# Kernel optimization log

Measured on AMD Instinct MI355X. Metric: run time of the kernel, lower is better.

The kernel has to match this reference:

```python
import jax, jax.numpy as jnp
import numpy as np

BASE_ALPHA = 0.05
NUM_ITER = 2
EPS = 1e-06


def setup_inputs() -> dict:
    key = jax.random.key(0)
    k1, k2 = jax.random.split(key)
    pred = jax.random.normal(k1, (8, 8192, 3), dtype=jnp.float32)
    partial = jax.random.normal(k2, (8, 2048, 3), dtype=jnp.float32)
    return {"pred": pred, "partial": partial}


def _cdist(a, b):
    # Euclidean pairwise distances via ||a||^2 - 2ab + ||b||^2 (avoids [B,N,M,3] temp).
    a2 = jnp.sum(a * a, axis=-1)  # [B,N]
    b2 = jnp.sum(b * b, axis=-1)  # [B,M]
    d2 = a2[:, :, None] - 2.0 * jnp.einsum('bnd,bmd->bnm', a, b) + b2[:, None, :]
    return jnp.sqrt(jnp.maximum(d2, 0.0))


def reference(pred, partial):
    refined = pred
    for _ in range(NUM_ITER):
        dist = _cdist(refined, partial)          # [B,N,M]
        min_dist = jnp.min(dist, axis=-1)        # [B,N]
        min_idx = jnp.argmin(dist, axis=-1)      # [B,N]
        nearest = jnp.take_along_axis(partial, min_idx[:, :, None], axis=1)  # [B,N,3]
        dist_norm = min_dist / (jnp.max(min_dist, axis=-1, keepdims=True) + EPS)
        alpha = BASE_ALPHA * (2.0 - dist_norm)   # [B,N]
        refined = refined + alpha[:, :, None] * (nearest - refined)
    return refined
```

## Files before the change

kernel.cpp:

```cpp
#include <hip/hip_runtime.h>
#include <math.h>

#define BATCH 8
#define NPRED 8192
#define MPART 2048
#define NPTS  (BATCH * NPRED)
#define MTOT  (BATCH * MPART)
#define QPL   4
#define SPLIT 16
#define PTS_PER_SPLIT (MPART / SPLIT)
#define GPS   (PTS_PER_SPLIT / 4)
#define QPB   256
#define NBLK  (NPTS / QPB)
#define BLK_PER_B (NPRED / QPB)
#define BASE_ALPHA 0.05f
#define EPS 1e-6f

__global__ __launch_bounds__(256) void prep_kernel(const float* __restrict__ partial,
                                                   float* __restrict__ ppgf,
                                                   float4* __restrict__ near4) {
    const int m = blockIdx.x * 256 + threadIdx.x;
    const float* p = partial + 3u * (unsigned)m;
    const float x = p[0], y = p[1], z = p[2];
    const int g = m >> 2, c = m & 3;
    float* base = ppgf + (size_t)g * 16 + c;
    base[0]  = -2.0f * x;
    base[4]  = -2.0f * y;
    base[8]  = -2.0f * z;
    base[12] = fmaf(x, x, fmaf(y, y, z * z));
    near4[m] = make_float4(x, y, z, 0.0f);
}

template <bool FUSE>
__global__ __launch_bounds__(1024) void nn_kernel(
    const float* __restrict__ src,
    const float4* __restrict__ ppg,
    const float4* __restrict__ near4,
    const float* md_in, const int* idx_in,
    const float* __restrict__ bmax_in,
    float* __restrict__ refined_out,
    float* md_out, int* idx_out,
    float* __restrict__ bmax_out)
{
    __shared__ float4 ldsP[2048];
    __shared__ float smax[4];
    unsigned long long* lk = (unsigned long long*)ldsP;

    const int qb   = blockIdx.x;
    const int b    = qb >> 5;
    const int tid  = threadIdx.x;
    const int wave = tid >> 6, lane = tid & 63;
    const int split = wave;

    const float4* gsrc = ppg + ((size_t)b << 11);
    ldsP[tid]        = gsrc[tid];
    ldsP[tid + 1024] = gsrc[tid + 1024];

    float axq[QPL], ayq[QPL], azq[QPL], a2q[QPL];
    if (FUSE) {
        float v = bmax_in[(b << 5) + (lane & 31)];
        #pragma unroll
        for (int o = 32; o > 0; o >>= 1) v = fmaxf(v, __shfl_down(v, o, 64));
        const float maxv = __shfl(v, 0, 64);
        #pragma unroll
        for (int j = 0; j < QPL; ++j) {
            const int t = (qb << 8) + (j << 6) + lane;
            const float md = md_in[t];
            const int   id = idx_in[t];
            const float alpha = BASE_ALPHA * (2.0f - md / (maxv + EPS));
            const float4 nb = near4[((size_t)b << 11) + id];
            const float* p = src + 3u * (unsigned)t;
            const float px = p[0], py = p[1], pz = p[2];
            axq[j] = fmaf(alpha, nb.x - px, px);
            ayq[j] = fmaf(alpha, nb.y - py, py);
            azq[j] = fmaf(alpha, nb.z - pz, pz);
            if (split == 0) {
                float* o = refined_out + 3u * (unsigned)t;
                o[0] = axq[j]; o[1] = ayq[j]; o[2] = azq[j];
            }
        }
    } else {
        #pragma unroll
        for (int j = 0; j < QPL; ++j) {
            const int t = (qb << 8) + (j << 6) + lane;
            const float* p = src + 3u * (unsigned)t;
            axq[j] = p[0]; ayq[j] = p[1]; azq[j] = p[2];
        }
    }
    #pragma unroll
    for (int j = 0; j < QPL; ++j)
        a2q[j] = fmaf(axq[j], axq[j], fmaf(ayq[j], ayq[j], azq[j] * azq[j]));

    __syncthreads();

    const float4* wp = ldsP + split * (GPS * 4);
    float best[QPL]; int bg[QPL];
    #pragma unroll
    for (int j = 0; j < QPL; ++j) { best[j] = 1e30f; bg[j] = 0; }

    #pragma unroll 2
    for (int i = 0; i < GPS; ++i) {
        const float4 X = wp[4 * i + 0];
        const float4 Y = wp[4 * i + 1];
        const float4 Z = wp[4 * i + 2];
        const float4 W = wp[4 * i + 3];
        #pragma unroll
        for (int j = 0; j < QPL; ++j) {
            const float ax = axq[j], ay = ayq[j], az = azq[j];
            const float d0 = fmaf(Z.x, az, fmaf(Y.x, ay, X.x * ax)) + W.x;
            const float d1 = fmaf(Z.y, az, fmaf(Y.y, ay, X.y * ax)) + W.y;
            const float d2 = fmaf(Z.z, az, fmaf(Y.z, ay, X.z * ax)) + W.z;
            const float d3 = fmaf(Z.w, az, fmaf(Y.w, ay, X.w * ax)) + W.w;
            const float gm = fminf(fminf(fminf(d0, d1), d2), d3);
            if (gm < best[j]) bg[j] = i;
            best[j] = fminf(best[j], gm);
        }
    }

    unsigned long long key[QPL];
    #pragma unroll
    for (int j = 0; j < QPL; ++j) {
        const int gi = bg[j];
        const float4 X = wp[4 * gi + 0];
        const float4 Y = wp[4 * gi + 1];
        const float4 Z = wp[4 * gi + 2];
        const float4 W = wp[4 * gi + 3];
        const float ax = axq[j], ay = ayq[j], az = azq[j];
        const float d0 = fmaf(Z.x, az, fmaf(Y.x, ay, X.x * ax)) + W.x;
        const float d1 = fmaf(Z.y, az, fmaf(Y.y, ay, X.y * ax)) + W.y;
        const float d2 = fmaf(Z.z, az, fmaf(Y.z, ay, X.z * ax)) + W.z;
        const float bv = best[j];
        int c;
        if      (d0 == bv) c = 0;
        else if (d1 == bv) c = 1;
        else if (d2 == bv) c = 2;
        else               c = 3;
        const int m = (split << 7) + (gi << 2) + c;
        const float dd = fmaxf(bv + a2q[j], 0.0f);
        key[j] = ((unsigned long long)__float_as_uint(dd) << 32) | (unsigned)m;
    }

    __syncthreads();
    #pragma unroll
    for (int j = 0; j < QPL; ++j)
        lk[split * QPB + (j << 6) + lane] = key[j];
    __syncthreads();

    if (wave < 4) {
        const int q2 = (wave << 6) + lane;
        unsigned long long kk = lk[q2];
        #pragma unroll
        for (int s = 1; s < SPLIT; ++s) {
            const unsigned long long k = lk[s * QPB + q2];
            if (k < kk) kk = k;
        }
        const float md = sqrtf(__uint_as_float((unsigned)(kk >> 32)));
        const int t2 = (qb << 8) + q2;
        md_out[t2]  = md;
        idx_out[t2] = (int)(kk & 0xffffffffu);
        float w = md;
        #pragma unroll
        for (int o = 32; o > 0; o >>= 1) w = fmaxf(w, __shfl_down(w, o, 64));
        if (lane == 0) smax[wave] = w;
    }
    __syncthreads();
    if (tid == 0)
        bmax_out[qb] = fmaxf(fmaxf(smax[0], smax[1]), fmaxf(smax[2], smax[3]));
}

__global__ __launch_bounds__(256) void update_kernel(
    const float* __restrict__ refined1,
    const float4* __restrict__ near4,
    const float* __restrict__ md2,
    const int*   __restrict__ idx2,
    const float* __restrict__ bmax2,
    float* __restrict__ out)
{
    const int t = blockIdx.x * 256 + threadIdx.x;
    const int b = t >> 13;
    const int lane = threadIdx.x & 63;
    float v = bmax2[(b << 5) + (lane & 31)];
    #pragma unroll
    for (int o = 32; o > 0; o >>= 1) v = fmaxf(v, __shfl_down(v, o, 64));
    const float maxv = __shfl(v, 0, 64);
    const float md = md2[t];
    const int   id = idx2[t];
    const float alpha = BASE_ALPHA * (2.0f - md / (maxv + EPS));
    const float4 nb = near4[((size_t)b << 11) + id];
    const float* p = refined1 + 3u * (unsigned)t;
    const float px = p[0], py = p[1], pz = p[2];
    float* o = out + 3u * (unsigned)t;
    o[0] = fmaf(alpha, nb.x - px, px);
    o[1] = fmaf(alpha, nb.y - py, py);
    o[2] = fmaf(alpha, nb.z - pz, pz);
}

extern "C" void kernel_launch(void* const* d_in, const int* in_sizes, int n_in,
                              void* d_out, int out_size, void* d_ws, size_t ws_size,
                              hipStream_t stream) {
    const float* pred    = (const float*)d_in[0];
    const float* partial = (const float*)d_in[1];
    float* out = (float*)d_out;

    char* ws = (char*)d_ws;
    float4* ppg   = (float4*)ws;
    float4* near4 = (float4*)(ws + 262144);
    float*  ref1  = (float*)(ws + 524288);
    float*  md1   = (float*)(ws + 1310720);
    int*    idx1  = (int*)(ws + 1572864);
    float*  bmax1 = (float*)(ws + 1835008);
    float*  bmax2 = bmax1 + NBLK;

    prep_kernel<<<MTOT / 256, 256, 0, stream>>>(partial, (float*)ppg, near4);

    nn_kernel<false><<<NBLK, 1024, 0, stream>>>(
        pred, ppg, near4, nullptr, nullptr, nullptr, nullptr, md1, idx1, bmax1);

    nn_kernel<true><<<NBLK, 1024, 0, stream>>>(
        pred, ppg, near4, md1, idx1, bmax1, ref1, md1, idx1, bmax2);

    update_kernel<<<NPTS / 256, 256, 0, stream>>>(ref1, near4, md1, idx1, bmax2, out);
}
```

Measured before the change: 99.25 us.

## Split NN search across two half-tile blocks and add key-combine kernel

Each nearest-neighbour block now uses 512 threads and scans half of the partial-cloud points, so twice as many smaller blocks run with a smaller LDS tile. A launch bound asks for four blocks per CU to raise occupancy. Per-half packed distance/index keys go to global memory, and a new combine kernel takes the min and computes per-block max distances. This adds two extra launches and a key round trip through global memory in exchange for better occupancy and load balance. The distance arithmetic is also refolded into a pure FMA chain with a tree min.

```diff
diff --git a/kernel.cpp b/kernel.cpp
--- a/kernel.cpp
+++ b/kernel.cpp
@@ -7,12 +7,11 @@
 #define NPTS  (BATCH * NPRED)
 #define MTOT  (BATCH * MPART)
 #define QPL   4
-#define SPLIT 16
-#define PTS_PER_SPLIT (MPART / SPLIT)
-#define GPS   (PTS_PER_SPLIT / 4)
 #define QPB   256
-#define NBLK  (NPTS / QPB)
-#define BLK_PER_B (NPRED / QPB)
+#define WAVES 8
+#define GPW   32
+#define NNBLK (2 * NPTS / QPB)
+#define NCMB  (NPTS / 1024)
 #define BASE_ALPHA 0.05f
 #define EPS 1e-6f
 
@@ -32,33 +31,32 @@
 }
 
 template <bool FUSE>
-__global__ __launch_bounds__(1024) void nn_kernel(
+__global__ __launch_bounds__(512, 4) void nn_kernel(
     const float* __restrict__ src,
     const float4* __restrict__ ppg,
     const float4* __restrict__ near4,
-    const float* md_in, const int* idx_in,
+    const float* __restrict__ md_in,
+    const int*   __restrict__ idx_in,
     const float* __restrict__ bmax_in,
-    float* __restrict__ refined_out,
-    float* md_out, int* idx_out,
-    float* __restrict__ bmax_out)
+    float* __restrict__ ref_out,
+    unsigned long long* __restrict__ keys_out)
 {
-    __shared__ float4 ldsP[2048];
-    __shared__ float smax[4];
-    unsigned long long* lk = (unsigned long long*)ldsP;
-
-    const int qb   = blockIdx.x;
+    __shared__ float4 tile[1024];
+    unsigned long long* lk = (unsigned long long*)tile;
+
+    const int qb   = blockIdx.x >> 1;
+    const int half = blockIdx.x & 1;
     const int b    = qb >> 5;
     const int tid  = threadIdx.x;
     const int wave = tid >> 6, lane = tid & 63;
-    const int split = wave;
-
-    const float4* gsrc = ppg + ((size_t)b << 11);
-    ldsP[tid]        = gsrc[tid];
-    ldsP[tid + 1024] = gsrc[tid + 1024];
+
+    const float4* gsrc = ppg + ((b << 11) + (half << 10));
+    tile[tid]       = gsrc[tid];
+    tile[tid + 512] = gsrc[tid + 512];
 
     float axq[QPL], ayq[QPL], azq[QPL], a2q[QPL];
     if (FUSE) {
-        float v = bmax_in[(b << 5) + (lane & 31)];
+        float v = bmax_in[(b << 3) + (lane & 7)];
         #pragma unroll
         for (int o = 32; o > 0; o >>= 1) v = fmaxf(v, __shfl_down(v, o, 64));
         const float maxv = __shfl(v, 0, 64);
@@ -68,14 +66,14 @@
             const float md = md_in[t];
             const int   id = idx_in[t];
             const float alpha = BASE_ALPHA * (2.0f - md / (maxv + EPS));
-            const float4 nb = near4[((size_t)b << 11) + id];
+            const float4 nb = near4[(b << 11) + id];
             const float* p = src + 3u * (unsigned)t;
             const float px = p[0], py = p[1], pz = p[2];
             axq[j] = fmaf(alpha, nb.x - px, px);
             ayq[j] = fmaf(alpha, nb.y - py, py);
             azq[j] = fmaf(alpha, nb.z - pz, pz);
-            if (split == 0) {
-                float* o = refined_out + 3u * (unsigned)t;
+            if (half == 0 && wave == 0) {
+                float* o = ref_out + 3u * (unsigned)t;
                 o[0] = axq[j]; o[1] = ayq[j]; o[2] = azq[j];
             }
         }
@@ -93,13 +91,13 @@
 
     __syncthreads();
 
-    const float4* wp = ldsP + split * (GPS * 4);
+    const float4* wp = tile + (wave << 7);
     float best[QPL]; int bg[QPL];
     #pragma unroll
     for (int j = 0; j < QPL; ++j) { best[j] = 1e30f; bg[j] = 0; }
 
-    #pragma unroll 2
-    for (int i = 0; i < GPS; ++i) {
+    #pragma unroll 4
+    for (int i = 0; i < GPW; ++i) {
         const float4 X = wp[4 * i + 0];
         const float4 Y = wp[4 * i + 1];
         const float4 Z = wp[4 * i + 2];
@@ -107,11 +105,11 @@
         #pragma unroll
         for (int j = 0; j < QPL; ++j) {
             const float ax = axq[j], ay = ayq[j], az = azq[j];
-            const float d0 = fmaf(Z.x, az, fmaf(Y.x, ay, X.x * ax)) + W.x;
-            const float d1 = fmaf(Z.y, az, fmaf(Y.y, ay, X.y * ax)) + W.y;
-            const float d2 = fmaf(Z.z, az, fmaf(Y.z, ay, X.z * ax)) + W.z;
-            const float d3 = fmaf(Z.w, az, fmaf(Y.w, ay, X.w * ax)) + W.w;
-            const float gm = fminf(fminf(fminf(d0, d1), d2), d3);
+            const float d0 = fmaf(Z.x, az, fmaf(Y.x, ay, fmaf(X.x, ax, W.x)));
+            const float d1 = fmaf(Z.y, az, fmaf(Y.y, ay, fmaf(X.y, ax, W.y)));
+            const float d2 = fmaf(Z.z, az, fmaf(Y.z, ay, fmaf(X.z, ax, W.z)));
+            const float d3 = fmaf(Z.w, az, fmaf(Y.w, ay, fmaf(X.w, ax, W.w)));
+            const float gm = fminf(fminf(d0, d1), fminf(d2, d3));
             if (gm < best[j]) bg[j] = i;
             best[j] = fminf(best[j], gm);
         }
@@ -126,16 +124,16 @@
         const float4 Z = wp[4 * gi + 2];
         const float4 W = wp[4 * gi + 3];
         const float ax = axq[j], ay = ayq[j], az = azq[j];
-        const float d0 = fmaf(Z.x, az, fmaf(Y.x, ay, X.x * ax)) + W.x;
-        const float d1 = fmaf(Z.y, az, fmaf(Y.y, ay, X.y * ax)) + W.y;
-        const float d2 = fmaf(Z.z, az, fmaf(Y.z, ay, X.z * ax)) + W.z;
+        const float d0 = fmaf(Z.x, az, fmaf(Y.x, ay, fmaf(X.x, ax, W.x)));
+        const float d1 = fmaf(Z.y, az, fmaf(Y.y, ay, fmaf(X.y, ax, W.y)));
+        const float d2 = fmaf(Z.z, az, fmaf(Y.z, ay, fmaf(X.z, ax, W.z)));
         const float bv = best[j];
         int c;
         if      (d0 == bv) c = 0;
         else if (d1 == bv) c = 1;
         else if (d2 == bv) c = 2;
         else               c = 3;
-        const int m = (split << 7) + (gi << 2) + c;
+        const int m = (half << 10) + (wave << 7) + (gi << 2) + c;
         const float dd = fmaxf(bv + a2q[j], 0.0f);
         key[j] = ((unsigned long long)__float_as_uint(dd) << 32) | (unsigned)m;
     }
@@ -143,33 +141,49 @@
     __syncthreads();
     #pragma unroll
     for (int j = 0; j < QPL; ++j)
-        lk[split * QPB + (j << 6) + lane] = key[j];
+        lk[wave * QPB + (j << 6) + lane] = key[j];
     __syncthreads();
 
     if (wave < 4) {
         const int q2 = (wave << 6) + lane;
         unsigned long long kk = lk[q2];
         #pragma unroll
-        for (int s = 1; s < SPLIT; ++s) {
+        for (int s = 1; s < WAVES; ++s) {
             const unsigned long long k = lk[s * QPB + q2];
             if (k < kk) kk = k;
         }
-        const float md = sqrtf(__uint_as_float((unsigned)(kk >> 32)));
-        const int t2 = (qb << 8) + q2;
-        md_out[t2]  = md;
-        idx_out[t2] = (int)(kk & 0xffffffffu);
-        float w = md;
-        #pragma unroll
-        for (int o = 32; o > 0; o >>= 1) w = fmaxf(w, __shfl_down(w, o, 64));
-        if (lane == 0) smax[wave] = w;
-    }
-    __syncthreads();
-    if (tid == 0)
-        bmax_out[qb] = fmaxf(fmaxf(smax[0], smax[1]), fmaxf(smax[2], smax[3]));
+        keys_out[half * NPTS + (qb << 8) + q2] = kk;
+    }
+}
+
+__global__ __launch_bounds__(1024) void combine_kernel(
+    const unsigned long long* __restrict__ keys,
+    float* __restrict__ md_out, int* __restrict__ idx_out,
+    float* __restrict__ bmax_out)
+{
+    __shared__ float smax[16];
+    const int t = blockIdx.x * 1024 + threadIdx.x;
+    const int wave = threadIdx.x >> 6, lane = threadIdx.x & 63;
+    const unsigned long long k0 = keys[t], k1 = keys[NPTS + t];
+    const unsigned long long kk = (k1 < k0) ? k1 : k0;
+    const float md = sqrtf(__uint_as_float((unsigned)(kk >> 32)));
+    md_out[t]  = md;
+    idx_out[t] = (int)(kk & 0xffffffffu);
+    float w = md;
+    #pragma unroll
+    for (int o = 32; o > 0; o >>= 1) w = fmaxf(w, __shfl_down(w, o, 64));
+    if (lane == 0) smax[wave] = w;
+    __syncthreads();
+    if (threadIdx.x < 64) {
+        float v = smax[lane & 15];
+        #pragma unroll
+        for (int o = 32; o > 0; o >>= 1) v = fmaxf(v, __shfl_down(v, o, 64));
+        if (lane == 0) bmax_out[blockIdx.x] = v;
+    }
 }
 
 __global__ __launch_bounds__(256) void update_kernel(
-    const float* __restrict__ refined1,
+    const float* __restrict__ ref1,
     const float4* __restrict__ near4,
     const float* __restrict__ md2,
     const int*   __restrict__ idx2,
@@ -179,15 +193,15 @@
     const int t = blockIdx.x * 256 + threadIdx.x;
     const int b = t >> 13;
     const int lane = threadIdx.x & 63;
-    float v = bmax2[(b << 5) + (lane & 31)];
+    float v = bmax2[(b << 3) + (lane & 7)];
     #pragma unroll
     for (int o = 32; o > 0; o >>= 1) v = fmaxf(v, __shfl_down(v, o, 64));
     const float maxv = __shfl(v, 0, 64);
     const float md = md2[t];
     const int   id = idx2[t];
     const float alpha = BASE_ALPHA * (2.0f - md / (maxv + EPS));
-    const float4 nb = near4[((size_t)b << 11) + id];
-    const float* p = refined1 + 3u * (unsigned)t;
+    const float4 nb = near4[(b << 11) + id];
+    const float* p = ref1 + 3u * (unsigned)t;
     const float px = p[0], py = p[1], pz = p[2];
     float* o = out + 3u * (unsigned)t;
     o[0] = fmaf(alpha, nb.x - px, px);
@@ -208,16 +222,19 @@
     float*  ref1  = (float*)(ws + 524288);
     float*  md1   = (float*)(ws + 1310720);
     int*    idx1  = (int*)(ws + 1572864);
-    float*  bmax1 = (float*)(ws + 1835008);
-    float*  bmax2 = bmax1 + NBLK;
+    unsigned long long* keys = (unsigned long long*)(ws + 1835008);
+    float*  bmax1 = (float*)(ws + 2883584);
+    float*  bmax2 = bmax1 + NCMB;
 
     prep_kernel<<<MTOT / 256, 256, 0, stream>>>(partial, (float*)ppg, near4);
 
-    nn_kernel<false><<<NBLK, 1024, 0, stream>>>(
-        pred, ppg, near4, nullptr, nullptr, nullptr, nullptr, md1, idx1, bmax1);
-
-    nn_kernel<true><<<NBLK, 1024, 0, stream>>>(
-        pred, ppg, near4, md1, idx1, bmax1, ref1, md1, idx1, bmax2);
+    nn_kernel<false><<<NNBLK, 512, 0, stream>>>(
+        pred, ppg, near4, nullptr, nullptr, nullptr, nullptr, keys);
+    combine_kernel<<<NCMB, 1024, 0, stream>>>(keys, md1, idx1, bmax1);
+
+    nn_kernel<true><<<NNBLK, 512, 0, stream>>>(
+        pred, ppg, near4, md1, idx1, bmax1, ref1, keys);
+    combine_kernel<<<NCMB, 1024, 0, stream>>>(keys, md1, idx1, bmax2);
 
     update_kernel<<<NPTS / 256, 256, 0, stream>>>(ref1, near4, md1, idx1, bmax2, out);
 }
```

Measured after the change: 100.7 us. No clear change (+1.4%).

## Fuse both NN iterations and final update into one cooperative kernel with grid sync

Applied to the files above, without the earlier changes.

Replaces the two nn_kernel launches and the update kernel with a single cooperative kernel. It keeps the partial tile and the refined query points resident in LDS and registers, and uses grid.sync for the per-batch max reductions. This removes two kernel launches and the global round-trips for md/idx/refined intermediates. It requires all 256 blocks of 1024 threads to be co-resident (launch_bounds 1024,4) and adds grid-wide barrier cost. LDS use per block rises to 64KB.

```diff
diff --git a/kernel.cpp b/kernel.cpp
--- a/kernel.cpp
+++ b/kernel.cpp
@@ -1,18 +1,14 @@
 #include <hip/hip_runtime.h>
+#include <hip/hip_cooperative_groups.h>
 #include <math.h>
+
+namespace cg = cooperative_groups;
 
 #define BATCH 8
 #define NPRED 8192
 #define MPART 2048
 #define NPTS  (BATCH * NPRED)
 #define MTOT  (BATCH * MPART)
-#define QPL   4
-#define SPLIT 16
-#define PTS_PER_SPLIT (MPART / SPLIT)
-#define GPS   (PTS_PER_SPLIT / 4)
-#define QPB   256
-#define NBLK  (NPTS / QPB)
-#define BLK_PER_B (NPRED / QPB)
 #define BASE_ALPHA 0.05f
 #define EPS 1e-6f
 
@@ -31,168 +27,165 @@
     near4[m] = make_float4(x, y, z, 0.0f);
 }
 
-template <bool FUSE>
-__global__ __launch_bounds__(1024) void nn_kernel(
-    const float* __restrict__ src,
+__global__ __launch_bounds__(1024, 4) void fused_kernel(
+    const float* __restrict__ pred,
     const float4* __restrict__ ppg,
     const float4* __restrict__ near4,
-    const float* md_in, const int* idx_in,
-    const float* __restrict__ bmax_in,
-    float* __restrict__ refined_out,
-    float* md_out, int* idx_out,
-    float* __restrict__ bmax_out)
+    float* __restrict__ bp1,
+    float* __restrict__ bp2,
+    float* __restrict__ out)
 {
-    __shared__ float4 ldsP[2048];
-    __shared__ float smax[4];
-    unsigned long long* lk = (unsigned long long*)ldsP;
+    cg::grid_group grid = cg::this_grid();
+
+    __shared__ float4 tile[2048];
+    __shared__ unsigned long long lk[4096];
 
     const int qb   = blockIdx.x;
     const int b    = qb >> 5;
     const int tid  = threadIdx.x;
     const int wave = tid >> 6, lane = tid & 63;
-    const int split = wave;
-
-    const float4* gsrc = ppg + ((size_t)b << 11);
-    ldsP[tid]        = gsrc[tid];
-    ldsP[tid + 1024] = gsrc[tid + 1024];
-
-    float axq[QPL], ayq[QPL], azq[QPL], a2q[QPL];
-    if (FUSE) {
-        float v = bmax_in[(b << 5) + (lane & 31)];
+
+    const float4* gsrc = ppg + (b << 11);
+    tile[tid]        = gsrc[tid];
+    tile[tid + 1024] = gsrc[tid + 1024];
+
+    float ax[4], ay[4], az[4], a2[4];
+    #pragma unroll
+    for (int j = 0; j < 4; ++j) {
+        const int t = (qb << 8) + (j << 6) + lane;
+        const float* p = pred + 3u * (unsigned)t;
+        ax[j] = p[0]; ay[j] = p[1]; az[j] = p[2];
+        a2[j] = fmaf(ax[j], ax[j], fmaf(ay[j], ay[j], az[j] * az[j]));
+    }
+    __syncthreads();
+
+    const float4* wp = tile + (wave << 7);
+
+    auto scan_keys = [&](unsigned long long* key) {
+        float best[4]; int bg[4];
+        #pragma unroll
+        for (int j = 0; j < 4; ++j) { best[j] = 1e30f; bg[j] = 0; }
+        #pragma unroll 4
+        for (int i = 0; i < 32; ++i) {
+            const float4 X = wp[4 * i + 0];
+            const float4 Y = wp[4 * i + 1];
+            const float4 Z = wp[4 * i + 2];
+            const float4 W = wp[4 * i + 3];
+            #pragma unroll
+            for (int j = 0; j < 4; ++j) {
+                const float d0 = fmaf(Z.x, az[j], fmaf(Y.x, ay[j], fmaf(X.x, ax[j], W.x)));
+                const float d1 = fmaf(Z.y, az[j], fmaf(Y.y, ay[j], fmaf(X.y, ax[j], W.y)));
+                const float d2 = fmaf(Z.z, az[j], fmaf(Y.z, ay[j], fmaf(X.z, ax[j], W.z)));
+                const float d3 = fmaf(Z.w, az[j], fmaf(Y.w, ay[j], fmaf(X.w, ax[j], W.w)));
+                const float gm = fminf(fminf(d0, d1), fminf(d2, d3));
+                if (gm < best[j]) bg[j] = i;
+                best[j] = fminf(best[j], gm);
+            }
+        }
+        #pragma unroll
+        for (int j = 0; j < 4; ++j) {
+            const int gi = bg[j];
+            const float4 X = wp[4 * gi + 0];
+            const float4 Y = wp[4 * gi + 1];
+            const float4 Z = wp[4 * gi + 2];
+            const float4 W = wp[4 * gi + 3];
+            const float d0 = fmaf(Z.x, az[j], fmaf(Y.x, ay[j], fmaf(X.x, ax[j], W.x)));
+            const float d1 = fmaf(Z.y, az[j], fmaf(Y.y, ay[j], fmaf(X.y, ax[j], W.y)));
+            const float d2 = fmaf(Z.z, az[j], fmaf(Y.z, ay[j], fmaf(X.z, ax[j], W.z)));
+            const float bv = best[j];
+            int c;
+            if      (d0 == bv) c = 0;
+            else if (d1 == bv) c = 1;
+            else if (d2 == bv) c = 2;
+            else               c = 3;
+            const int m = (wave << 7) + (gi << 2) + c;
+            const float dd = fmaxf(bv + a2[j], 0.0f);
+            key[j] = ((unsigned long long)__float_as_uint(dd) << 32) | (unsigned)m;
+        }
+    };
+
+    unsigned long long key1[4];
+    scan_keys(key1);
+    #pragma unroll
+    for (int j = 0; j < 4; ++j)
+        lk[(wave << 8) + (j << 6) + lane] = key1[j];
+    __syncthreads();
+
+    if (tid < 256) {
+        unsigned long long kk = lk[tid];
+        #pragma unroll
+        for (int s = 1; s < 16; ++s) {
+            const unsigned long long k = lk[(s << 8) + tid];
+            if (k < kk) kk = k;
+        }
+        lk[tid] = kk;
+        float w = sqrtf(__uint_as_float((unsigned)(kk >> 32)));
+        #pragma unroll
+        for (int o = 32; o > 0; o >>= 1) w = fmaxf(w, __shfl_down(w, o, 64));
+        if (lane == 0) bp1[(qb << 2) + wave] = w;
+    }
+    grid.sync();
+
+    {
+        float v = fmaxf(bp1[(b << 7) + lane], bp1[(b << 7) + 64 + lane]);
         #pragma unroll
         for (int o = 32; o > 0; o >>= 1) v = fmaxf(v, __shfl_down(v, o, 64));
         const float maxv = __shfl(v, 0, 64);
-        #pragma unroll
-        for (int j = 0; j < QPL; ++j) {
-            const int t = (qb << 8) + (j << 6) + lane;
-            const float md = md_in[t];
-            const int   id = idx_in[t];
+
+        #pragma unroll
+        for (int j = 0; j < 4; ++j) {
+            const int q = (j << 6) + lane;
+            const unsigned long long kk = lk[q];
+            const float md = sqrtf(__uint_as_float((unsigned)(kk >> 32)));
+            const int   id = (int)(kk & 0xffffffffu);
             const float alpha = BASE_ALPHA * (2.0f - md / (maxv + EPS));
-            const float4 nb = near4[((size_t)b << 11) + id];
-            const float* p = src + 3u * (unsigned)t;
-            const float px = p[0], py = p[1], pz = p[2];
-            axq[j] = fmaf(alpha, nb.x - px, px);
-            ayq[j] = fmaf(alpha, nb.y - py, py);
-            azq[j] = fmaf(alpha, nb.z - pz, pz);
-            if (split == 0) {
-                float* o = refined_out + 3u * (unsigned)t;
-                o[0] = axq[j]; o[1] = ayq[j]; o[2] = azq[j];
-            }
-        }
-    } else {
-        #pragma unroll
-        for (int j = 0; j < QPL; ++j) {
-            const int t = (qb << 8) + (j << 6) + lane;
-            const float* p = src + 3u * (unsigned)t;
-            axq[j] = p[0]; ayq[j] = p[1]; azq[j] = p[2];
-        }
-    }
+            const float4 nb = near4[(b << 11) + id];
+            ax[j] = fmaf(alpha, nb.x - ax[j], ax[j]);
+            ay[j] = fmaf(alpha, nb.y - ay[j], ay[j]);
+            az[j] = fmaf(alpha, nb.z - az[j], az[j]);
+            a2[j] = fmaf(ax[j], ax[j], fmaf(ay[j], ay[j], az[j] * az[j]));
+        }
+    }
+    __syncthreads();
+
+    unsigned long long key2[4];
+    scan_keys(key2);
     #pragma unroll
-    for (int j = 0; j < QPL; ++j)
-        a2q[j] = fmaf(axq[j], axq[j], fmaf(ayq[j], ayq[j], azq[j] * azq[j]));
-
-    __syncthreads();
-
-    const float4* wp = ldsP + split * (GPS * 4);
-    float best[QPL]; int bg[QPL];
-    #pragma unroll
-    for (int j = 0; j < QPL; ++j) { best[j] = 1e30f; bg[j] = 0; }
-
-    #pragma unroll 2
-    for (int i = 0; i < GPS; ++i) {
-        const float4 X = wp[4 * i + 0];
-        const float4 Y = wp[4 * i + 1];
-        const float4 Z = wp[4 * i + 2];
-        const float4 W = wp[4 * i + 3];
-        #pragma unroll
-        for (int j = 0; j < QPL; ++j) {
-            const float ax = axq[j], ay = ayq[j], az = azq[j];
-            const float d0 = fmaf(Z.x, az, fmaf(Y.x, ay, X.x * ax)) + W.x;
-            const float d1 = fmaf(Z.y, az, fmaf(Y.y, ay, X.y * ax)) + W.y;
-            const float d2 = fmaf(Z.z, az, fmaf(Y.z, ay, X.z * ax)) + W.z;
-            const float d3 = fmaf(Z.w, az, fmaf(Y.w, ay, X.w * ax)) + W.w;
-            const float gm = fminf(fminf(fminf(d0, d1), d2), d3);
-            if (gm < best[j]) bg[j] = i;
-            best[j] = fminf(best[j], gm);
-        }
-    }
-
-    unsigned long long key[QPL];
-    #pragma unroll
-    for (int j = 0; j < QPL; ++j) {
-        const int gi = bg[j];
-        const float4 X = wp[4 * gi + 0];
-        const float4 Y = wp[4 * gi + 1];
-        const float4 Z = wp[4 * gi + 2];
-        const float4 W = wp[4 * gi + 3];
-        const float ax = axq[j], ay = ayq[j], az = azq[j];
-        const float d0 = fmaf(Z.x, az, fmaf(Y.x, ay, X.x * ax)) + W.x;
-        const float d1 = fmaf(Z.y, az, fmaf(Y.y, ay, X.y * ax)) + W.y;
-        const float d2 = fmaf(Z.z, az, fmaf(Y.z, ay, X.z * ax)) + W.z;
-        const float bv = best[j];
-        int c;
-        if      (d0 == bv) c = 0;
-        else if (d1 == bv) c = 1;
-        else if (d2 == bv) c = 2;
-        else               c = 3;
-        const int m = (split << 7) + (gi << 2) + c;
-        const float dd = fmaxf(bv + a2q[j], 0.0f);
-        key[j] = ((unsigned long long)__float_as_uint(dd) << 32) | (unsigned)m;
-    }
-
-    __syncthreads();
-    #pragma unroll
-    for (int j = 0; j < QPL; ++j)
-        lk[split * QPB + (j << 6) + lane] = key[j];
-    __syncthreads();
-
-    if (wave < 4) {
-        const int q2 = (wave << 6) + lane;
-        unsigned long long kk = lk[q2];
-        #pragma unroll
-        for (int s = 1; s < SPLIT; ++s) {
-            const unsigned long long k = lk[s * QPB + q2];
+    for (int j = 0; j < 4; ++j)
+        lk[(wave << 8) + (j << 6) + lane] = key2[j];
+    __syncthreads();
+
+    float md2 = 0.0f; int idx2 = 0;
+    if (tid < 256) {
+        unsigned long long kk = lk[tid];
+        #pragma unroll
+        for (int s = 1; s < 16; ++s) {
+            const unsigned long long k = lk[(s << 8) + tid];
             if (k < kk) kk = k;
         }
-        const float md = sqrtf(__uint_as_float((unsigned)(kk >> 32)));
-        const int t2 = (qb << 8) + q2;
-        md_out[t2]  = md;
-        idx_out[t2] = (int)(kk & 0xffffffffu);
-        float w = md;
+        md2  = sqrtf(__uint_as_float((unsigned)(kk >> 32)));
+        idx2 = (int)(kk & 0xffffffffu);
+        float w = md2;
         #pragma unroll
         for (int o = 32; o > 0; o >>= 1) w = fmaxf(w, __shfl_down(w, o, 64));
-        if (lane == 0) smax[wave] = w;
-    }
-    __syncthreads();
-    if (tid == 0)
-        bmax_out[qb] = fmaxf(fmaxf(smax[0], smax[1]), fmaxf(smax[2], smax[3]));
-}
-
-__global__ __launch_bounds__(256) void update_kernel(
-    const float* __restrict__ refined1,
-    const float4* __restrict__ near4,
-    const float* __restrict__ md2,
-    const int*   __restrict__ idx2,
-    const float* __restrict__ bmax2,
-    float* __restrict__ out)
-{
-    const int t = blockIdx.x * 256 + threadIdx.x;
-    const int b = t >> 13;
-    const int lane = threadIdx.x & 63;
-    float v = bmax2[(b << 5) + (lane & 31)];
-    #pragma unroll
-    for (int o = 32; o > 0; o >>= 1) v = fmaxf(v, __shfl_down(v, o, 64));
-    const float maxv = __shfl(v, 0, 64);
-    const float md = md2[t];
-    const int   id = idx2[t];
-    const float alpha = BASE_ALPHA * (2.0f - md / (maxv + EPS));
-    const float4 nb = near4[((size_t)b << 11) + id];
-    const float* p = refined1 + 3u * (unsigned)t;
-    const float px = p[0], py = p[1], pz = p[2];
-    float* o = out + 3u * (unsigned)t;
-    o[0] = fmaf(alpha, nb.x - px, px);
-    o[1] = fmaf(alpha, nb.y - py, py);
-    o[2] = fmaf(alpha, nb.z - pz, pz);
+        if (lane == 0) bp2[(qb << 2) + wave] = w;
+    }
+    grid.sync();
+
+    if (tid < 256) {
+        float v = fmaxf(bp2[(b << 7) + lane], bp2[(b << 7) + 64 + lane]);
+        #pragma unroll
+        for (int o = 32; o > 0; o >>= 1) v = fmaxf(v, __shfl_down(v, o, 64));
+        const float maxv = __shfl(v, 0, 64);
+        const float alpha = BASE_ALPHA * (2.0f - md2 / (maxv + EPS));
+        const float4 nb = near4[(b << 11) + idx2];
+        const int j = wave;
+        const float px = ax[j], py = ay[j], pz = az[j];
+        float* o = out + 3u * (unsigned)((qb << 8) + tid);
+        o[0] = fmaf(alpha, nb.x - px, px);
+        o[1] = fmaf(alpha, nb.y - py, py);
+        o[2] = fmaf(alpha, nb.z - pz, pz);
+    }
 }
 
 extern "C" void kernel_launch(void* const* d_in, const int* in_sizes, int n_in,
@@ -205,19 +198,13 @@
     char* ws = (char*)d_ws;
     float4* ppg   = (float4*)ws;
     float4* near4 = (float4*)(ws + 262144);
-    float*  ref1  = (float*)(ws + 524288);
-    float*  md1   = (float*)(ws + 1310720);
-    int*    idx1  = (int*)(ws + 1572864);
-    float*  bmax1 = (float*)(ws + 1835008);
-    float*  bmax2 = bmax1 + NBLK;
+    float*  bp1   = (float*)(ws + 524288);
+    float*  bp2   = (float*)(ws + 528384);
 
     prep_kernel<<<MTOT / 256, 256, 0, stream>>>(partial, (float*)ppg, near4);
 
-    nn_kernel<false><<<NBLK, 1024, 0, stream>>>(
-        pred, ppg, near4, nullptr, nullptr, nullptr, nullptr, md1, idx1, bmax1);
-
-    nn_kernel<true><<<NBLK, 1024, 0, stream>>>(
-        pred, ppg, near4, md1, idx1, bmax1, ref1, md1, idx1, bmax2);
-
-    update_kernel<<<NPTS / 256, 256, 0, stream>>>(ref1, near4, md1, idx1, bmax2, out);
+    void* args[] = { (void*)&pred, (void*)&ppg, (void*)&near4,
+                     (void*)&bp1, (void*)&bp2, (void*)&out };
+    hipLaunchCooperativeKernel((void*)fused_kernel, dim3(256), dim3(1024),
+                               args, 0, stream);
 }
```

Result: slower. 151.2 us (+52.4%).
